# Kernel optimization log

Hardware: AMD Instinct MI355X
Metric: run time of the kernel (lower is better)

## Reference

```python
import jax, jax.numpy as jnp
import numpy as np

N_FFT = 1024
HOP = 256
WIN_LEN = N_FFT  # win_length == n_fft
PAD = (WIN_LEN - HOP) // 2  # 'same' padding


def hann_window(n):
    # torch.hann_window default (periodic=True): 0.5*(1-cos(2*pi*k/n))
    k = jnp.arange(n, dtype=jnp.float32)
    return 0.5 * (1.0 - jnp.cos(2.0 * jnp.pi * k / n))


def setup_inputs() -> dict:
    key = jax.random.key(0)
    k1, k2 = jax.random.split(key)
    B, L, D = 8, 2048, 512
    x = jax.random.normal(k1, (B, L, D), dtype=jnp.float32)
    W = jax.random.normal(k2, (D, N_FFT + 2), dtype=jnp.float32) * (1.0 / np.sqrt(D))
    b = jnp.zeros((N_FFT + 2,), dtype=jnp.float32)
    return {"x": x, "W": W, "b": b}


def reference(x, W, b):
    # Linear projection: (B, L, n_fft+2)
    h = jnp.einsum("bld,do->blo", x, W) + b
    nbins = N_FFT // 2 + 1  # 513
    mag = jnp.minimum(jnp.exp(h[..., :nbins]), 100.0)  # exp + clip max=100
    p = h[..., nbins:]
    # Complex STFT coefficients S: (B, L, nbins)
    S = mag * (jnp.cos(p) + 1j * jnp.sin(p))
    # Per-frame inverse rFFT (norm='backward' = default): (B, L, n_fft)
    frames = jnp.fft.irfft(S, n=N_FFT, axis=-1)
    win = hann_window(WIN_LEN)
    frames = frames * win  # windowed frames
    B, T = frames.shape[0], frames.shape[1]
    out_size = (T - 1) * HOP + WIN_LEN
    # Overlap-add via scatter-add
    idx = jnp.arange(T)[:, None] * HOP + jnp.arange(WIN_LEN)[None, :]  # (T, n_fft)
    y = jnp.zeros((B, out_size), dtype=frames.dtype).at[:, idx].add(frames)
    env = jnp.zeros((out_size,), dtype=frames.dtype).at[idx].add(
        jnp.broadcast_to(win * win, (T, WIN_LEN))
    )
    y = y[:, PAD:-PAD] / env[PAD:-PAD]
    return y
```

## Files before the change

### kernel.cpp

```cpp
#include <hip/hip_runtime.h>
#include <math.h>


using half8 = __attribute__((ext_vector_type(8))) _Float16;
using f32x4 = __attribute__((ext_vector_type(4))) float;

#define TWO_PI_OVER_1024 0.006135923151542565f

#define OFF_A2 0
#define OFF_B2 35651584UL
#define OFF_A1 37879808UL
#define OFF_B1 54657024UL
#define OFF_FL 37879808UL
#define OFF_FH 56754176UL

__device__ __forceinline__ float hannf(int s) {
    return 0.5f * (1.0f - __cosf(TWO_PI_OVER_1024 * (float)s));
}

__device__ __forceinline__ void stage16(const void* g, void* lds) {
    __builtin_amdgcn_global_load_lds(
        (const __attribute__((address_space(1))) void*)g,
        (__attribute__((address_space(3))) void*)lds,
        16, 0, 0);
}

__global__ __launch_bounds__(256)
void prep_k(const float* __restrict__ x, const float* __restrict__ W,
            _Float16* __restrict__ A1, _Float16* __restrict__ B1,
            _Float16* __restrict__ B2)
{
    const int bid = blockIdx.x;
    if (bid < 4096) {
        const size_t tid = (size_t)bid * 256 + threadIdx.x;
        const int l   = (int)(tid & 63);
        const size_t f = tid >> 6;
        const int mts = (int)(f & 7);
        const size_t g = f >> 3;
        const int kt  = (int)(g & 15);
        const int mtb = (int)(g >> 4);
        const int m   = mtb * 128 + mts * 16 + (l & 15);
        const int k0  = kt * 32 + (l >> 4) * 8;
        const float* xp = x + (size_t)m * 512 + k0;
        const float4 v0 = *(const float4*)xp;
        const float4 v1 = *(const float4*)(xp + 4);
        const float vv[8] = {v0.x, v0.y, v0.z, v0.w, v1.x, v1.y, v1.z, v1.w};
        half8 o;
#pragma unroll
        for (int j = 0; j < 8; ++j) o[j] = (_Float16)vv[j];
        *(half8*)(A1 + tid * 8) = o;
    } else if (bid < 4384) {
        const int tid = (bid - 4096) * 256 + threadIdx.x;
        const int l  = tid & 63;
        const int f  = tid >> 6;
        const int t8 = f & 7;
        const int g  = f >> 3;
        const int kt = g & 15;
        const int bx = g >> 4;
        const int side = t8 >> 2;
        const int nt   = t8 & 3;
        const int c    = bx * 64 + nt * 16 + (l & 15);
        const int k0   = kt * 32 + (l >> 4) * 8;
        const int wcol = side ? (513 + c) : c;
        half8 o;
#pragma unroll
        for (int j = 0; j < 8; ++j) {
            float v = (c < 513) ? W[(size_t)(k0 + j) * 1026 + wcol] : 0.0f;
            o[j] = (_Float16)v;
        }
        *(half8*)(B1 + (size_t)tid * 8) = o;
    } else {
        const int tid = (bid - 4384) * 256 + threadIdx.x;
        const int l  = tid & 63;
        const int f  = tid >> 6;
        const int nt = f % 6;
        const int g  = f / 6;
        const int kt = g % 34;
        const int nblk = g / 34;
        const int n  = nblk * 96 + nt * 16 + (l & 15);
        const int kk0 = kt * 32 + (l >> 4) * 8;
        const float win = hannf(n) * (1.0f / 1024.0f);
        half8 o;
#pragma unroll
        for (int j = 0; j < 8; ++j) {
            const int kk = kk0 + j;
            float v = 0.0f;
            if (kk < 544) {
                const int k = kk;
                if (k < 513) {
                    const float coef = (k == 0 || k == 512) ? 1.0f : 2.0f;
                    v = coef * __cosf(TWO_PI_OVER_1024 * (float)((k * n) & 1023)) * win;
                }
            } else {
                const int k = kk - 544;
                if (k < 513) {
                    const float coef = (k == 0 || k == 512) ? 1.0f : 2.0f;
                    v = -coef * __sinf(TWO_PI_OVER_1024 * (float)((k * n) & 1023)) * win;
                }
            }
            o[j] = (_Float16)v;
        }
        *(half8*)(B2 + (size_t)tid * 8) = o;
    }
}


__global__ __launch_bounds__(256, 4)
void gemm1_k(const _Float16* __restrict__ A, const _Float16* __restrict__ B,
             const float* __restrict__ bias, _Float16* __restrict__ A2)
{
    __shared__ _Float16 Ash[2][8 * 512];
    __shared__ _Float16 Bsh[2][8 * 512];
    const int t = threadIdx.x, w = t >> 6, l = t & 63;

    const int lin = blockIdx.x;
    const int xcd = lin & 7, slot = lin >> 3;
    const int mblk = xcd * 16 + slot / 9;
    const int bx   = slot % 9;

    const int wm = (w & 1) * 4;
    const int q  = w >> 1;
    const int jt[4] = {2 * q, 2 * q + 1, 4 + 2 * q, 5 + 2 * q};

    f32x4 acc[4][4];
#pragma unroll
    for (int i = 0; i < 4; ++i)
#pragma unroll
        for (int j = 0; j < 4; ++j) acc[i][j] = (f32x4)0.0f;

    const int lane8 = l * 8;
    const _Float16* Ab = A + ((size_t)mblk * 16 * 8) * 512 + lane8;
    const _Float16* Bb = B + ((size_t)bx * 16 * 8) * 512 + lane8;

    for (int step = 0; step < 8; ++step) {
        const int kt0 = 2 * step;
        __syncthreads();
#pragma unroll
        for (int i = 0; i < 4; ++i) {
            const int s = 4 * w + i;
            const int u = s >> 3, r = s & 7;
            stage16(Ab + ((size_t)(kt0 + u) * 8 + r) * 512, &Ash[u][r * 512]);
            stage16(Bb + ((size_t)(kt0 + u) * 8 + r) * 512, &Bsh[u][r * 512]);
        }
        __syncthreads();

#pragma unroll
        for (int u = 0; u < 2; ++u) {
            half8 a[4], b[4];
#pragma unroll
            for (int i = 0; i < 4; ++i)
                a[i] = *(const half8*)&Ash[u][(wm + i) * 512 + lane8];
#pragma unroll
            for (int j = 0; j < 4; ++j)
                b[j] = *(const half8*)&Bsh[u][jt[j] * 512 + lane8];
#pragma unroll
            for (int i = 0; i < 4; ++i)
#pragma unroll
                for (int j = 0; j < 4; ++j)
                    acc[i][j] = __builtin_amdgcn_mfma_f32_16x16x32_f16(a[i], b[j], acc[i][j], 0, 0, 0);
        }
    }

    _Float16* SrT = &Ash[0][0];
    _Float16* SiT = &Bsh[0][0];

    __syncthreads();
    const int r4 = (l >> 4) * 4, c16 = l & 15;
#pragma unroll
    for (int i = 0; i < 4; ++i) {
        const int row0 = (wm + i) * 16 + r4;
#pragma unroll
        for (int p = 0; p < 2; ++p) {
            const int cl = (2 * q + p) * 16 + c16;
            const int c  = bx * 64 + cl;
            const bool valid = (c < 513);
            const float bm = valid ? bias[c] : 0.0f;
            const float bp = valid ? bias[513 + c] : 0.0f;
#pragma unroll
            for (int r = 0; r < 4; ++r) {
                float Sr = 0.0f, Si = 0.0f;
                if (valid) {
                    const float mag = fminf(__expf(acc[i][p][r] + bm), 100.0f);
                    const float ph  = acc[i][2 + p][r] + bp;
                    Sr = mag * __cosf(ph);
                    Si = mag * __sinf(ph);
                }
                const int row = row0 + r;
                const int idx = row * 64 + (cl ^ ((row & 7) * 8));
                SrT[idx] = (_Float16)Sr;
                SiT[idx] = (_Float16)Si;
            }
        }
    }
    __syncthreads();

#pragma unroll
    for (int f = 0; f < 4; ++f) {
        const int tau  = w * 4 + f;
        const int kt2l = tau >> 3, mts = tau & 7;
        if (bx * 2 + kt2l < 17) {
            const int row = mts * 16 + (l & 15);
            const int kl  = kt2l * 32 + (l >> 4) * 8;
            const int idx = row * 64 + (kl ^ ((row & 7) * 8));
            const half8 vr = *(const half8*)&SrT[idx];
            const half8 vi = *(const half8*)&SiT[idx];
            const int ktr = bx * 2 + kt2l;
            const int kti = 17 + ktr;
            *(half8*)(A2 + ((((size_t)mblk * 34 + ktr) * 8 + mts) * 64 + l) * 8) = vr;
            *(half8*)(A2 + ((((size_t)mblk * 34 + kti) * 8 + mts) * 64 + l) * 8) = vi;
        }
    }
}


__device__ __forceinline__ void mma43(const _Float16* __restrict__ As,
                                      const _Float16* __restrict__ Bs,
                                      int wm, int wn, int lane16, f32x4 (&acc)[4][3])
{
    half8 a[4], b[3];
#pragma unroll
    for (int i = 0; i < 4; ++i) a[i] = *(const half8*)&As[(wm + i) * 512 + lane16];
#pragma unroll
    for (int j = 0; j < 3; ++j) b[j] = *(const half8*)&Bs[(wn + j) * 512 + lane16];
#pragma unroll
    for (int i = 0; i < 4; ++i)
#pragma unroll
        for (int j = 0; j < 3; ++j)
            acc[i][j] = __builtin_amdgcn_mfma_f32_16x16x32_f16(a[i], b[j], acc[i][j], 0, 0, 0);
}

__global__ __launch_bounds__(256, 3)
void gemm2_k(const _Float16* __restrict__ A, const _Float16* __restrict__ Bas,
             _Float16* __restrict__ FL, _Float16* __restrict__ FH)
{
    __shared__ _Float16 SH[14336];
    _Float16* As0 = SH;
    _Float16* Bs0 = SH + 8192;
    const int t = threadIdx.x, w = t >> 6, l = t & 63;

    const int lin = blockIdx.x;
    const int xcd = lin & 7, slot = lin >> 3;
    const int mblk = xcd * 16 + slot / 6;
    const int nblk = slot % 6;

    const int wm = (w & 1) * 4, wn = (w >> 1) * 3;

    f32x4 accC[4][3], accD[4][3];
#pragma unroll
    for (int i = 0; i < 4; ++i)
#pragma unroll
        for (int j = 0; j < 3; ++j) { accC[i][j] = (f32x4)0.0f; accD[i][j] = (f32x4)0.0f; }

    const int lane16 = l * 8;

    for (int step = 0; step < 17; ++step) {
        const int kt0 = 2 * step;
        __syncthreads();
#pragma unroll
        for (int i = 0; i < 4; ++i) {
            const int ta = 4 * w + i;
            const int u = ta >> 3, mts = ta & 7;
            const _Float16* Ag = A + ((((size_t)mblk * 34 + (kt0 + u)) * 8 + mts) * 512) + lane16;
            stage16(Ag, &As0[u * 4096 + mts * 512]);
        }
#pragma unroll
        for (int i = 0; i < 3; ++i) {
            const int tb = 3 * w + i;
            const int u = tb / 6, nt = tb % 6;
            const _Float16* Bg = Bas + ((((size_t)nblk * 34 + (kt0 + u)) * 6 + nt) * 512) + lane16;
            stage16(Bg, &Bs0[u * 3072 + nt * 512]);
        }
        __syncthreads();

#pragma unroll
        for (int u = 0; u < 2; ++u) {
            const int kt = kt0 + u;
            if (kt < 17) mma43(As0 + u * 4096, Bs0 + u * 3072, wm, wn, lane16, accC);
            else         mma43(As0 + u * 4096, Bs0 + u * 3072, wm, wn, lane16, accD);
        }
    }

    const int r4 = (l >> 4) * 4, c0 = l & 15;
    __syncthreads();
#pragma unroll
    for (int i = 0; i < 4; ++i) {
        const int row = (wm + i) * 16 + r4;
#pragma unroll
        for (int j = 0; j < 3; ++j) {
            const int lcol = (wn + j) * 16 + c0;
#pragma unroll
            for (int r = 0; r < 4; ++r)
                SH[(row + r) * 104 + lcol] = (_Float16)(accC[i][j][r] + accD[i][j][r]);
        }
    }
    __syncthreads();
    for (int qq = t; qq < 1536; qq += 256) {
        const int row = qq / 12, cc = qq % 12;
        const half8 v = *(const half8*)&SH[row * 104 + cc * 8];
        *(half8*)(FL + (size_t)(mblk * 128 + row) * 576 + nblk * 96 + cc * 8) = v;
    }
    __syncthreads();

    const int Cbase = (nblk == 5) ? 0 : (416 - 96 * nblk);
    const int lo = (nblk == 5) ? 0 : 1;
    const int hi = (nblk == 0) ? 95 : ((nblk == 5) ? 32 : 96);
#pragma unroll
    for (int i = 0; i < 4; ++i) {
        const int row = (wm + i) * 16 + r4;
#pragma unroll
        for (int j = 0; j < 3; ++j) {
            const int n = nblk * 96 + (wn + j) * 16 + c0;
#pragma unroll
            for (int r = 0; r < 4; ++r) {
                if (n >= 1 && n <= 511)
                    SH[(row + r) * 104 + (512 - n - Cbase)] =
                        (_Float16)(accC[i][j][r] - accD[i][j][r]);
                else if (n == 512)
                    SH[(row + r) * 104 + 0] =
                        (_Float16)(accC[i][j][r] + accD[i][j][r]);
            }
        }
    }
    __syncthreads();
    for (int qq = t; qq < 1664; qq += 256) {
        const int row = qq / 13, cc = qq % 13;
        if (8 * cc > hi) continue;
        _Float16* dst = FH + (size_t)(mblk * 128 + row) * 512 + Cbase + 8 * cc;
        if (8 * cc >= lo && 8 * cc + 7 <= hi) {
            *(half8*)dst = *(const half8*)&SH[row * 104 + cc * 8];
        } else {
#pragma unroll
            for (int e = 0; e < 8; ++e) {
                const int lc = 8 * cc + e;
                if (lc >= lo && lc <= hi) dst[e] = SH[row * 104 + lc];
            }
        }
    }
}


__global__ __launch_bounds__(256)
void ola_kernel(const _Float16* __restrict__ FL, const _Float16* __restrict__ FH,
                float* __restrict__ out)
{
    const int gid = blockIdx.x * 256 + threadIdx.x;
    const size_t base = (size_t)gid * 8;
    const int b  = (int)(base >> 19);
    const int j0 = (int)(base & 524287);
    const int n0 = j0 + 384;

    if (j0 >= 640 && j0 < 523904) {
        const int nb = n0 & 255;
        const int T  = n0 >> 8;
        const size_t mT = (size_t)b * 2048 + T;
        const half8 v0 = *(const half8*)(FL + (mT    ) * 576 + nb);
        const half8 v1 = *(const half8*)(FL + (mT - 1) * 576 + nb + 256);
        const half8 v2 = *(const half8*)(FH + (mT - 2) * 512 + nb);
        const half8 v3 = *(const half8*)(FH + (mT - 3) * 512 + nb + 256);
        f32x4 o0, o1;
#pragma unroll
        for (int e = 0; e < 4; ++e)
            o0[e] = ((float)v0[e] + (float)v1[e] + (float)v2[e] + (float)v3[e]) * (2.0f / 3.0f);
#pragma unroll
        for (int e = 0; e < 4; ++e)
            o1[e] = ((float)v0[4 + e] + (float)v1[4 + e] + (float)v2[4 + e] + (float)v3[4 + e]) * (2.0f / 3.0f);
        *(f32x4*)(out + base) = o0;
        *(f32x4*)(out + base + 4) = o1;
    } else {
        for (int e = 0; e < 8; ++e) {
            const int n = n0 + e;
            int t_hi = n >> 8;
            if (t_hi > 2047) t_hi = 2047;
            const int t_lo = (n >= 1023) ? ((n - 768) >> 8) : 0;
            float acc = 0.0f, env = 0.0f;
            for (int tt = t_lo; tt <= t_hi; ++tt) {
                const int s = n - (tt << 8);
                const float wv = hannf(s);
                const size_t m = (size_t)b * 2048 + tt;
                const float fv = (s < 512) ? (float)FL[m * 576 + s]
                                           : (float)FH[m * 512 + (s - 512)];
                acc += fv;
                env += wv * wv;
            }
            out[base + e] = acc / env;
        }
    }
}


extern "C" void kernel_launch(void* const* d_in, const int* in_sizes, int n_in,
                              void* d_out, int out_size, void* d_ws, size_t ws_size,
                              hipStream_t stream)
{
    const float* x = (const float*)d_in[0];
    const float* W = (const float*)d_in[1];
    const float* b = (const float*)d_in[2];
    float* out = (float*)d_out;
    char* ws = (char*)d_ws;

    _Float16* A2 = (_Float16*)(ws + OFF_A2);
    _Float16* B2 = (_Float16*)(ws + OFF_B2);
    _Float16* A1 = (_Float16*)(ws + OFF_A1);
    _Float16* B1 = (_Float16*)(ws + OFF_B1);
    _Float16* FL = (_Float16*)(ws + OFF_FL);
    _Float16* FH = (_Float16*)(ws + OFF_FH);

    prep_k<<<4690, 256, 0, stream>>>(x, W, A1, B1, B2);

    gemm1_k<<<1152, 256, 0, stream>>>(A1, B1, b, A2);
    gemm2_k<<<768, 256, 0, stream>>>(A2, B2, FL, FH);

    ola_kernel<<<out_size / 2048, 256, 0, stream>>>(FL, FH, out);
}
```

Before: 164.9 us.

## Double-buffer LDS staging in both GEMM kernels to overlap loads with MFMA

Both GEMM main loops change from staging two K-tiles and then computing them, to a ping-pong scheme. The next K-tile is issued with global_load_lds into the alternate buffer while MFMAs run on the current one, with a single barrier per iteration. The aim is to hide global-to-LDS latency behind compute. In exchange there are twice as many barriers, since each iteration now covers one tile instead of two. Correctness also relies on the barrier at the end of each iteration to make the async LDS loads visible before the next tile is read.

```diff
diff --git a/kernel.cpp b/kernel.cpp
--- a/kernel.cpp
+++ b/kernel.cpp
@@ -109,8 +109,8 @@
 void gemm1_k(const _Float16* __restrict__ A, const _Float16* __restrict__ B,
              const float* __restrict__ bias, _Float16* __restrict__ A2)
 {
-    __shared__ _Float16 Ash[2][8 * 512];
-    __shared__ _Float16 Bsh[2][8 * 512];
+    __shared__ _Float16 Ash[2][4096];
+    __shared__ _Float16 Bsh[2][4096];
     const int t = threadIdx.x, w = t >> 6, l = t & 63;
 
     const int lin = blockIdx.x;
@@ -129,42 +129,49 @@
         for (int j = 0; j < 4; ++j) acc[i][j] = (f32x4)0.0f;
 
     const int lane8 = l * 8;
-    const _Float16* Ab = A + ((size_t)mblk * 16 * 8) * 512 + lane8;
-    const _Float16* Bb = B + ((size_t)bx * 16 * 8) * 512 + lane8;
-
-    for (int step = 0; step < 8; ++step) {
-        const int kt0 = 2 * step;
+    const _Float16* Ab = A + ((size_t)mblk * 128) * 512 + lane8;
+    const _Float16* Bb = B + ((size_t)bx * 128) * 512 + lane8;
+
+#define STAGE1(kt, p)                                                        \
+    {                                                                        \
+        _Pragma("unroll")                                                    \
+        for (int i = 0; i < 4; ++i) {                                        \
+            const int s = 4 * w + i;                                         \
+            if (s < 8)                                                       \
+                stage16(Ab + ((size_t)(kt) * 8 + s) * 512, &Ash[p][s * 512]);\
+            else                                                             \
+                stage16(Bb + ((size_t)(kt) * 8 + (s - 8)) * 512,             \
+                        &Bsh[p][(s - 8) * 512]);                             \
+        }                                                                    \
+    }
+
+    STAGE1(0, 0);
+    __syncthreads();
+
+    for (int kt = 0; kt < 16; ++kt) {
+        const int p = kt & 1;
+        if (kt < 15) STAGE1(kt + 1, p ^ 1);
+
+        half8 a[4], b[4];
+#pragma unroll
+        for (int i = 0; i < 4; ++i)
+            a[i] = *(const half8*)&Ash[p][(wm + i) * 512 + lane8];
+#pragma unroll
+        for (int j = 0; j < 4; ++j)
+            b[j] = *(const half8*)&Bsh[p][jt[j] * 512 + lane8];
+#pragma unroll
+        for (int i = 0; i < 4; ++i)
+#pragma unroll
+            for (int j = 0; j < 4; ++j)
+                acc[i][j] = __builtin_amdgcn_mfma_f32_16x16x32_f16(a[i], b[j], acc[i][j], 0, 0, 0);
+
         __syncthreads();
-#pragma unroll
-        for (int i = 0; i < 4; ++i) {
-            const int s = 4 * w + i;
-            const int u = s >> 3, r = s & 7;
-            stage16(Ab + ((size_t)(kt0 + u) * 8 + r) * 512, &Ash[u][r * 512]);
-            stage16(Bb + ((size_t)(kt0 + u) * 8 + r) * 512, &Bsh[u][r * 512]);
-        }
-        __syncthreads();
-
-#pragma unroll
-        for (int u = 0; u < 2; ++u) {
-            half8 a[4], b[4];
-#pragma unroll
-            for (int i = 0; i < 4; ++i)
-                a[i] = *(const half8*)&Ash[u][(wm + i) * 512 + lane8];
-#pragma unroll
-            for (int j = 0; j < 4; ++j)
-                b[j] = *(const half8*)&Bsh[u][jt[j] * 512 + lane8];
-#pragma unroll
-            for (int i = 0; i < 4; ++i)
-#pragma unroll
-                for (int j = 0; j < 4; ++j)
-                    acc[i][j] = __builtin_amdgcn_mfma_f32_16x16x32_f16(a[i], b[j], acc[i][j], 0, 0, 0);
-        }
-    }
+    }
+#undef STAGE1
 
     _Float16* SrT = &Ash[0][0];
     _Float16* SiT = &Bsh[0][0];
 
-    __syncthreads();
     const int r4 = (l >> 4) * 4, c16 = l & 15;
 #pragma unroll
     for (int i = 0; i < 4; ++i) {
@@ -234,8 +241,6 @@
              _Float16* __restrict__ FL, _Float16* __restrict__ FH)
 {
     __shared__ _Float16 SH[14336];
-    _Float16* As0 = SH;
-    _Float16* Bs0 = SH + 8192;
     const int t = threadIdx.x, w = t >> 6, l = t & 63;
 
     const int lin = blockIdx.x;
@@ -253,35 +258,37 @@
 
     const int lane16 = l * 8;
 
-    for (int step = 0; step < 17; ++step) {
-        const int kt0 = 2 * step;
+#define STAGE2(kt, p)                                                          \
+    {                                                                          \
+        _Pragma("unroll")                                                      \
+        for (int i = 0; i < 4; ++i) {                                          \
+            const int s = i * 4 + w;                                           \
+            if (s < 8) {                                                       \
+                const _Float16* Ag =                                           \
+                    A + ((((size_t)mblk * 34 + (kt)) * 8 + s) * 512) + lane16; \
+                stage16(Ag, SH + (p) * 4096 + s * 512);                        \
+            } else if (s < 14) {                                               \
+                const int nt = s - 8;                                          \
+                const _Float16* Bg =                                           \
+                    Bas + ((((size_t)nblk * 34 + (kt)) * 6 + nt) * 512) + lane16; \
+                stage16(Bg, SH + 8192 + (p) * 3072 + nt * 512);                \
+            }                                                                  \
+        }                                                                      \
+    }
+
+    STAGE2(0, 0);
+    __syncthreads();
+
+    for (int kt = 0; kt < 34; ++kt) {
+        const int p = kt & 1;
+        if (kt < 33) STAGE2(kt + 1, p ^ 1);
+        if (kt < 17) mma43(SH + p * 4096, SH + 8192 + p * 3072, wm, wn, lane16, accC);
+        else         mma43(SH + p * 4096, SH + 8192 + p * 3072, wm, wn, lane16, accD);
         __syncthreads();
-#pragma unroll
-        for (int i = 0; i < 4; ++i) {
-            const int ta = 4 * w + i;
-            const int u = ta >> 3, mts = ta & 7;
-            const _Float16* Ag = A + ((((size_t)mblk * 34 + (kt0 + u)) * 8 + mts) * 512) + lane16;
-            stage16(Ag, &As0[u * 4096 + mts * 512]);
-        }
-#pragma unroll
-        for (int i = 0; i < 3; ++i) {
-            const int tb = 3 * w + i;
-            const int u = tb / 6, nt = tb % 6;
-            const _Float16* Bg = Bas + ((((size_t)nblk * 34 + (kt0 + u)) * 6 + nt) * 512) + lane16;
-            stage16(Bg, &Bs0[u * 3072 + nt * 512]);
-        }
-        __syncthreads();
-
-#pragma unroll
-        for (int u = 0; u < 2; ++u) {
-            const int kt = kt0 + u;
-            if (kt < 17) mma43(As0 + u * 4096, Bs0 + u * 3072, wm, wn, lane16, accC);
-            else         mma43(As0 + u * 4096, Bs0 + u * 3072, wm, wn, lane16, accD);
-        }
-    }
+    }
+#undef STAGE2
 
     const int r4 = (l >> 4) * 4, c0 = l & 15;
-    __syncthreads();
 #pragma unroll
     for (int i = 0; i < 4; ++i) {
         const int row = (wm + i) * 16 + r4;
```

New measurement: 177.2 us. +7.5%, slower.
